# Optimization experiments

Hardware: AMD Instinct MI355X
Metric: run time of the kernel (lower is better)

## Reference

```python
import jax, jax.numpy as jnp
import numpy as np

EPS = 1e-12

def _safe_norm(x, axis):
    return jnp.sqrt(jnp.sum(x * x, axis=axis) + EPS)

def _forward(z, pos, edge_index, batch, batch_size, emb, centers, gamma,
             fw1, fb1, fw2, fb2, uw1, ub1, uw2, ub2,
             ew1, eb1, ew2, eb2, dipole_w, nac_w,
             aw1, ab1, aw2, ab2, yw1, yb1, yw2, yb2):
    row, col = edge_index[0], edge_index[1]
    N = pos.shape[0]
    diff = pos[col] - pos[row]                    # (E,3)
    dist = _safe_norm(diff, axis=1)               # (E,)
    dirs = diff / (dist[:, None] + 1e-8)          # (E,3)
    rbf = jnp.exp(-gamma * (dist[:, None] - centers) ** 2)   # (E,R)
    s = emb[z]                                    # (N,F)
    v = jnp.zeros((N, s.shape[1], 3), s.dtype)    # (N,F,3)
    n_layers = fw1.shape[0]
    for l in range(n_layers):
        # filter MLP on RBF features -> 3 gates per edge
        phi = jax.nn.silu(rbf @ fw1[l] + fb1[l]) @ fw2[l] + fb2[l]   # (E,3F)
        phi_ss, phi_vv, phi_sv = jnp.split(phi, 3, axis=-1)
        sc = s[col]                                                    # gather (E,F)
        m_s = jax.ops.segment_sum(phi_ss * sc, row, num_segments=N)    # (N,F)
        m_v_e = (phi_vv[..., None] * v[col]
                 + phi_sv[..., None] * dirs[:, None, :] * sc[..., None])  # (E,F,3)
        m_v = jax.ops.segment_sum(m_v_e, row, num_segments=N)          # (N,F,3)
        v_norm = _safe_norm(m_v, axis=-1)                              # (N,F)
        upd = (jax.nn.silu(jnp.concatenate([s, m_s, v_norm], axis=-1) @ uw1[l] + ub1[l])
               @ uw2[l] + ub2[l])                                       # (N,3F)
        delta_s, alpha, beta = jnp.split(upd, 3, axis=-1)
        s = s + delta_s
        v = alpha[..., None] * v + beta[..., None] * m_v
    # energy heads (stacked over states S)
    h = jax.nn.silu(jnp.einsum('nf,sfg->nsg', s, ew1) + eb1)           # (N,S,F)
    e_atom = (jnp.einsum('nsg,sgo->nso', h, ew2) + eb2)[..., 0]        # (N,S)
    energies = jax.ops.segment_sum(e_atom, batch, num_segments=batch_size)  # (M,S)
    dipoles = jax.ops.segment_sum(jnp.einsum('nfk,f->nk', v, dipole_w), batch,
                                  num_segments=batch_size)             # (M,3)
    nac = jax.ops.segment_sum(jnp.einsum('nfk,pf->npk', v, nac_w), batch,
                              num_segments=batch_size)                 # (M,P,3)
    gaps = energies[:, 1:] - energies[:, :1]                           # (M,S-1)
    lam = jax.nn.silu(gaps @ aw1 + ab1) @ aw2 + ab2                    # (M,1)
    nac_mag = _safe_norm(nac, axis=-1)                                 # (M,P)
    phi_y = jax.nn.sigmoid(
        jax.nn.silu(jnp.concatenate([gaps, nac_mag], axis=1) @ yw1 + yb1) @ yw2 + yb2)  # (M,1)
    return energies, dipoles, nac, lam, phi_y

N, E, F, R, L, S, M, A = 20000, 320000, 128, 20, 3, 4, 1000, 100
P = S - 1

def setup_inputs() -> dict:
    key = jax.random.key(0)
    ks = jax.random.split(key, 32)
    w = lambda i, shape, sc=0.05: jax.random.normal(ks[i], shape, jnp.float32) * sc
    return {
        'z': jax.random.randint(ks[0], (N,), 0, A),
        'pos': jax.random.normal(ks[1], (N, 3), jnp.float32),
        'edge_index': jax.random.randint(ks[2], (2, E), 0, N),
        'batch': jnp.sort(jax.random.randint(ks[3], (N,), 0, M)),
        'batch_size': M,
        'emb': jax.random.normal(ks[4], (A, F), jnp.float32),
        'centers': jnp.linspace(0.0, 5.0, R),
        'gamma': jnp.ones((R,), jnp.float32),
        'fw1': w(5, (L, R, F)), 'fb1': jnp.zeros((L, F)),
        'fw2': w(6, (L, F, 3 * F)), 'fb2': jnp.zeros((L, 3 * F)),
        'uw1': w(7, (L, 3 * F, F)), 'ub1': jnp.zeros((L, F)),
        'uw2': w(8, (L, F, 3 * F)), 'ub2': jnp.zeros((L, 3 * F)),
        'ew1': w(9, (S, F, F)), 'eb1': jnp.zeros((S, F)),
        'ew2': w(10, (S, F, 1)), 'eb2': jnp.zeros((S, 1)),
        'dipole_w': jax.random.normal(ks[11], (F,), jnp.float32),
        'nac_w': jax.random.normal(ks[12], (P, F), jnp.float32),
        'aw1': w(13, (S - 1, 64)), 'ab1': jnp.zeros((64,)),
        'aw2': w(14, (64, 1)), 'ab2': jnp.zeros((1,)),
        'yw1': w(15, (S - 1 + P, 128)), 'yb1': jnp.zeros((128,)),
        'yw2': w(16, (128, 1)), 'yb2': jnp.zeros((1,)),
    }

def reference(z, pos, edge_index, batch, batch_size, emb, centers, gamma,
              fw1, fb1, fw2, fb2, uw1, ub1, uw2, ub2,
              ew1, eb1, ew2, eb2, dipole_w, nac_w,
              aw1, ab1, aw2, ab2, yw1, yb1, yw2, yb2):
    return _forward(z, pos, edge_index, batch, batch_size, emb, centers, gamma,
                    fw1, fb1, fw2, fb2, uw1, ub1, uw2, ub2,
                    ew1, eb1, ew2, eb2, dipole_w, nac_w,
                    aw1, ab1, aw2, ab2, yw1, yb1, yw2, yb2)
```

## Files before the change

kernel.cpp:

```cpp
#include <hip/hip_runtime.h>
#include <hip/hip_fp16.h>

#define FDIM 128
#define RDIM 20

#define TAB_T 2048
#define TAB_RANGE 12.0f

constexpr int TH = 256;

__device__ __forceinline__ float siluf(float x) { return x / (1.f + __expf(-x)); }

__device__ __forceinline__ void store_h4(__half* p, float a, float b, float c, float d) {
    __half h[4] = {__float2half(a), __float2half(b), __float2half(c), __float2half(d)};
    *(uint2*)p = *(uint2*)h;
}

__global__ void k_init(const int* __restrict__ z, const float* __restrict__ emb,
                       float* __restrict__ s, __half* __restrict__ s_h, int N) {
    int i = blockIdx.x * blockDim.x + threadIdx.x;
    if (i >= N * FDIM) return;
    int n = i >> 7, f = i & 127;
    float val = emb[z[n] * FDIM + f];
    s[i] = val;
    s_h[i] = __float2half(val);
}

__global__ void k_hist(const int* __restrict__ erow, int* __restrict__ cursor, int E) {
    int e = blockIdx.x * blockDim.x + threadIdx.x;
    if (e < E) atomicAdd(&cursor[erow[e]], 1);
}

__global__ __launch_bounds__(256) void k_scan1(const int* __restrict__ cursor,
                                               int* __restrict__ rowstart,
                                               int* __restrict__ bsum, int N) {
    __shared__ int sh[256];
    int tid = threadIdx.x;
    int idx = blockIdx.x * 256 + tid;
    int x = (idx < N) ? cursor[idx] : 0;
    sh[tid] = x;
    __syncthreads();
    #pragma unroll
    for (int off = 1; off < 256; off <<= 1) {
        int t = (tid >= off) ? sh[tid - off] : 0;
        __syncthreads();
        sh[tid] += t;
        __syncthreads();
    }
    if (idx < N) rowstart[idx] = sh[tid] - x;
    if (tid == 255) bsum[blockIdx.x] = sh[255];
}

__global__ __launch_bounds__(256) void k_scan2(int* __restrict__ bsum,
                                               int* __restrict__ rowstart, int nb, int N) {
    __shared__ int sh[256];
    __shared__ int carry;
    int tid = threadIdx.x;
    if (tid == 0) carry = 0;
    __syncthreads();
    for (int base = 0; base < nb; base += 256) {
        int idx = base + tid;
        int x = (idx < nb) ? bsum[idx] : 0;
        sh[tid] = x;
        __syncthreads();
        #pragma unroll
        for (int off = 1; off < 256; off <<= 1) {
            int t = (tid >= off) ? sh[tid - off] : 0;
            __syncthreads();
            sh[tid] += t;
            __syncthreads();
        }
        if (idx < nb) bsum[idx] = carry + sh[tid] - x;
        __syncthreads();
        if (tid == 0) carry += sh[255];
        __syncthreads();
    }
    if (tid == 0) rowstart[N] = carry;
}

__global__ __launch_bounds__(256) void k_scan3(int* __restrict__ rowstart,
                                               int* __restrict__ cursor,
                                               const int* __restrict__ bsum, int N) {
    int idx = blockIdx.x * 256 + threadIdx.x;
    if (idx < N) {
        int val = rowstart[idx] + bsum[blockIdx.x];
        rowstart[idx] = val;
        cursor[idx] = val;
    }
}

__global__ void k_fill(const int* __restrict__ erow, int* __restrict__ cursor,
                       int* __restrict__ esort, int E) {
    int e = blockIdx.x * blockDim.x + threadIdx.x;
    if (e < E) {
        int p = atomicAdd(&cursor[erow[e]], 1);
        esort[p] = e;
    }
}

__global__ void k_geom(const float* __restrict__ pos, const int* __restrict__ erow,
                       const int* __restrict__ ecol, const int* __restrict__ esort,
                       int2* __restrict__ geo_ci, float4* __restrict__ geo_wd,
                       float inv_step, int E) {
    int i = blockIdx.x * blockDim.x + threadIdx.x;
    if (i >= E) return;
    int e  = esort[i];
    int rw = erow[e], cl = ecol[e];
    float dx = pos[cl*3+0] - pos[rw*3+0];
    float dy = pos[cl*3+1] - pos[rw*3+1];
    float dz = pos[cl*3+2] - pos[rw*3+2];
    float dist = sqrtf(dx*dx + dy*dy + dz*dz + 1e-12f);
    float inv = 1.f / (dist + 1e-8f);
    float u = fminf(dist * inv_step, (float)TAB_T);
    int t0 = min((int)u, TAB_T - 1);
    geo_ci[i] = make_int2(cl, t0);
    geo_wd[i] = make_float4(u - (float)t0, dx*inv, dy*inv, dz*inv);
}

__global__ __launch_bounds__(TH) void k_table(
    const float* __restrict__ centers, const float* __restrict__ gamma,
    const float* __restrict__ fw1b, const float* __restrict__ fb1b,
    const float* __restrict__ fw2b, const float* __restrict__ fb2b,
    __half* __restrict__ tabb, float step)
{
    __shared__ float sh_rbf[32][RDIM];
    __shared__ float sh_ht[FDIM][33];
    __shared__ float sh_w[32][3 * FDIM + 4];

    const int l   = blockIdx.y;
    const float* fw1 = fw1b + (size_t)l * RDIM * FDIM;
    const float* fb1 = fb1b + (size_t)l * FDIM;
    const float* fw2 = fw2b + (size_t)l * FDIM * 3 * FDIM;
    const float* fb2 = fb2b + (size_t)l * 3 * FDIM;
    __half* tab = tabb + (size_t)l * (TAB_T + 1) * 384;

    const int p0  = blockIdx.x * 32;
    const int tid = threadIdx.x;

    for (int i = tid; i < 32 * RDIM; i += TH) {
        int p = i / RDIM, r = i - p * RDIM;
        float d = (float)(p0 + p) * step - centers[r];
        sh_rbf[p][r] = __expf(-gamma[r] * d * d);
    }
    __syncthreads();
    for (int i = tid; i < 32 * FDIM; i += TH) {
        int p = i >> 7, f = i & 127;
        float acc = fb1[f];
        #pragma unroll
        for (int r = 0; r < RDIM; ++r) acc += sh_rbf[p][r] * fw1[r * FDIM + f];
        sh_ht[f][p] = siluf(acc);
    }

    const int eq = tid & 7;
    const int fq = tid >> 3;
    const int f0 = fq * 4;

    float pg[3][4][4];
    #pragma unroll
    for (int g3 = 0; g3 < 3; ++g3)
        #pragma unroll
        for (int ee = 0; ee < 4; ++ee)
            #pragma unroll
            for (int i = 0; i < 4; ++i) pg[g3][ee][i] = fb2[g3 * FDIM + f0 + i];

    const int kkr = tid >> 3;
    const int t8  = tid & 7;
    for (int kc = 0; kc < 4; ++kc) {
        __syncthreads();
        #pragma unroll
        for (int j = 0; j < 12; ++j) {
            int g = (t8 * 12 + j) * 4;
            float4 w4 = *(const float4*)&fw2[(size_t)(kc * 32 + kkr) * (3 * FDIM) + g];
            *(float4*)&sh_w[kkr][g] = w4;
        }
        __syncthreads();
        #pragma unroll 4
        for (int kk = 0; kk < 32; ++kk) {
            float hv[4];
            #pragma unroll
            for (int ee = 0; ee < 4; ++ee) hv[ee] = sh_ht[kc * 32 + kk][4 * eq + ee];
            #pragma unroll
            for (int g3 = 0; g3 < 3; ++g3) {
                float4 w4 = *(const float4*)&sh_w[kk][g3 * FDIM + f0];
                #pragma unroll
                for (int ee = 0; ee < 4; ++ee) {
                    pg[g3][ee][0] += hv[ee] * w4.x;
                    pg[g3][ee][1] += hv[ee] * w4.y;
                    pg[g3][ee][2] += hv[ee] * w4.z;
                    pg[g3][ee][3] += hv[ee] * w4.w;
                }
            }
        }
    }

    #pragma unroll
    for (int ee = 0; ee < 4; ++ee) {
        int pt = p0 + 4 * eq + ee;
        if (pt <= TAB_T) {
            #pragma unroll
            for (int g3 = 0; g3 < 3; ++g3)
                store_h4(&tab[(size_t)pt * 384 + g3 * FDIM + f0],
                         pg[g3][ee][0], pg[g3][ee][1], pg[g3][ee][2], pg[g3][ee][3]);
        }
    }
}

__global__ __launch_bounds__(256) void k_repack(const __half* __restrict__ tab,
                                                __half2* __restrict__ tab2) {
    int l = blockIdx.y;
    const __half* t  = tab  + (size_t)l * (TAB_T + 1) * 384;
    __half2*      t2 = tab2 + (size_t)l * TAB_T * 384;
    int i = blockIdx.x * 256 + threadIdx.x;
    t2[i] = __halves2half2(t[i], t[i + 384]);
}

__global__ __launch_bounds__(128) void k_gather(
    const int* __restrict__ rowstart,
    const int2* __restrict__ geo_ci, const float4* __restrict__ geo_wd,
    const __half2* __restrict__ tab2, const __half* __restrict__ s_h,
    const __half* __restrict__ v_h,
    __half* __restrict__ m_s_h, __half* __restrict__ vnorm_h, __half* __restrict__ m_v_h,
    int withv, int N)
{
    __shared__ int   sh_col[32];
    __shared__ int   sh_t0[32];
    __shared__ float sh_w[32];
    __shared__ float sh_d0[32], sh_d1[32], sh_d2[32];

    const int n   = blockIdx.x;
    const int tid = threadIdx.x;
    const int lo  = rowstart[n], hi = rowstart[n + 1];

    float acc_s = 0.f, av0 = 0.f, av1 = 0.f, av2 = 0.f;

    for (int base = lo; base < hi; base += 32) {
        const int ne = min(32, hi - base);
        __syncthreads();
        if (tid < 32) {
            int idx = base + tid;
            if (tid < ne) {
                int2   ci = geo_ci[idx];
                float4 wd = geo_wd[idx];
                sh_col[tid] = ci.x; sh_t0[tid] = ci.y;
                sh_w[tid] = wd.x;
                sh_d0[tid] = wd.y; sh_d1[tid] = wd.z; sh_d2[tid] = wd.w;
            } else {
                sh_col[tid] = 0; sh_t0[tid] = 0; sh_w[tid] = 0.f;
                sh_d0[tid] = sh_d1[tid] = sh_d2[tid] = 0.f;
            }
        }
        __syncthreads();
        if (withv) {
            #pragma unroll 2
            for (int el = 0; el < ne; ++el) {
                int   cl = sh_col[el];
                int   t0 = sh_t0[el];
                float w  = sh_w[el];
                const __half2* t2 = tab2 + (size_t)t0 * 384 + tid;
                float2 pss2 = __half22float2(t2[0]);
                float2 pvv2 = __half22float2(t2[128]);
                float2 psv2 = __half22float2(t2[256]);
                float pss = pss2.x + w * (pss2.y - pss2.x);
                float pvv = pvv2.x + w * (pvv2.y - pvv2.x);
                float psv = psv2.x + w * (psv2.y - psv2.x);
                float sc = __half2float(s_h[(size_t)cl * FDIM + tid]);
                const __half* vp = v_h + (size_t)cl * 3 * FDIM + tid;
                float svs = psv * sc;
                acc_s += pss * sc;
                av0 += pvv * __half2float(vp[0])        + svs * sh_d0[el];
                av1 += pvv * __half2float(vp[FDIM])     + svs * sh_d1[el];
                av2 += pvv * __half2float(vp[2*FDIM])   + svs * sh_d2[el];
            }
        } else {
            #pragma unroll 2
            for (int el = 0; el < ne; ++el) {
                int   cl = sh_col[el];
                int   t0 = sh_t0[el];
                float w  = sh_w[el];
                const __half2* t2 = tab2 + (size_t)t0 * 384 + tid;
                float2 pss2 = __half22float2(t2[0]);
                float2 psv2 = __half22float2(t2[256]);
                float pss = pss2.x + w * (pss2.y - pss2.x);
                float psv = psv2.x + w * (psv2.y - psv2.x);
                float sc = __half2float(s_h[(size_t)cl * FDIM + tid]);
                float svs = psv * sc;
                acc_s += pss * sc;
                av0 += svs * sh_d0[el];
                av1 += svs * sh_d1[el];
                av2 += svs * sh_d2[el];
            }
        }
    }

    m_s_h[(size_t)n * FDIM + tid]  = __float2half(acc_s);
    vnorm_h[(size_t)n * FDIM + tid] = __float2half(sqrtf(av0*av0 + av1*av1 + av2*av2 + 1e-12f));
    __half* mh = m_v_h + (size_t)n * 3 * FDIM + tid;
    mh[0]      = __float2half(av0);
    mh[FDIM]   = __float2half(av1);
    mh[2*FDIM] = __float2half(av2);
}

__global__ __launch_bounds__(256) void k_mlp1(
    const __half* __restrict__ s_h, const __half* __restrict__ m_s_h,
    const __half* __restrict__ vnorm_h,
    const float* __restrict__ uw1, const float* __restrict__ ub1,
    __half* __restrict__ u1_h, int N)
{
    __shared__ float shA[16][36];
    __shared__ float shB[16][132];

    const int tid = threadIdx.x;
    const int n0  = blockIdx.x * 32;
    const int tx  = tid & 15, ty = tid >> 4;
    const int cA  = tx * 4, cB = 64 + tx * 4;
    const int r0  = ty * 2;
    const int rs  = (tid & 127) >> 2;
    const int k4  = (tid & 3) * 4;
    const int bk  = tid >> 5;
    const int bc4 = (tid & 31) * 4;

    float acc[2][8];
    {
        float4 bA = *(const float4*)&ub1[cA];
        float4 bB = *(const float4*)&ub1[cB];
        #pragma unroll
        for (int i = 0; i < 2; ++i) {
            acc[i][0]=bA.x; acc[i][1]=bA.y; acc[i][2]=bA.z; acc[i][3]=bA.w;
            acc[i][4]=bB.x; acc[i][5]=bB.y; acc[i][6]=bB.z; acc[i][7]=bB.w;
        }
    }

    uint2 pa; float4 pb0, pb1;

#define MLP1_LOAD(kc) do { \
        pa = make_uint2(0u, 0u); \
        if (tid < 128) { \
            int kg = (kc) * 16 + k4; int n = n0 + rs; \
            if (n < N) { \
                const __half* base; \
                if (kg < 128)      base = &s_h[(size_t)n * FDIM + kg]; \
                else if (kg < 256) base = &m_s_h[(size_t)n * FDIM + kg - 128]; \
                else               base = &vnorm_h[(size_t)n * FDIM + kg - 256]; \
                pa = *(const uint2*)base; \
            } \
        } \
        pb0 = *(const float4*)&uw1[(size_t)((kc)*16 + bk) * FDIM + bc4]; \
        pb1 = *(const float4*)&uw1[(size_t)((kc)*16 + 8 + bk) * FDIM + bc4]; \
    } while (0)

    MLP1_LOAD(0);
    for (int kc = 0; kc < 24; ++kc) {
        __syncthreads();
        if (tid < 128) {
            const __half* ph = (const __half*)&pa;
            shA[k4+0][rs] = __half2float(ph[0]); shA[k4+1][rs] = __half2float(ph[1]);
            shA[k4+2][rs] = __half2float(ph[2]); shA[k4+3][rs] = __half2float(ph[3]);
        }
        *(float4*)&shB[bk][bc4]     = pb0;
        *(float4*)&shB[8 + bk][bc4] = pb1;
        if (kc + 1 < 24) MLP1_LOAD(kc + 1);
        __syncthreads();
        #pragma unroll
        for (int kk = 0; kk < 16; ++kk) {
            float2 a2 = *(const float2*)&shA[kk][r0];
            float4 b0 = *(const float4*)&shB[kk][cA];
            float4 b1 = *(const float4*)&shB[kk][cB];
            float av[2] = {a2.x, a2.y};
            #pragma unroll
            for (int i = 0; i < 2; ++i) {
                acc[i][0] += av[i]*b0.x; acc[i][1] += av[i]*b0.y;
                acc[i][2] += av[i]*b0.z; acc[i][3] += av[i]*b0.w;
                acc[i][4] += av[i]*b1.x; acc[i][5] += av[i]*b1.y;
                acc[i][6] += av[i]*b1.z; acc[i][7] += av[i]*b1.w;
            }
        }
    }
#undef MLP1_LOAD

    #pragma unroll
    for (int i = 0; i < 2; ++i) {
        int n = n0 + r0 + i;
        if (n < N) {
            store_h4(&u1_h[(size_t)n * FDIM + cA],
                     siluf(acc[i][0]), siluf(acc[i][1]), siluf(acc[i][2]), siluf(acc[i][3]));
            store_h4(&u1_h[(size_t)n * FDIM + cB],
                     siluf(acc[i][4]), siluf(acc[i][5]), siluf(acc[i][6]), siluf(acc[i][7]));
        }
    }
}

__global__ __launch_bounds__(256) void k_mlp2(
    const __half* __restrict__ u1_h, const float* __restrict__ uw2, const float* __restrict__ ub2,
    float* __restrict__ s, __half* __restrict__ v_h, const __half* __restrict__ m_v_h,
    __half* __restrict__ s_h, int wmirror, int N)
{
    __shared__ float shU[32][132];
    __shared__ float shB[16][132];

    const int tid = threadIdx.x;
    const int n0  = blockIdx.x * 32;
    const int tx  = tid & 15, ty = tid >> 4;
    const int cA  = tx * 4, cB = 64 + tx * 4;
    const int r0  = ty * 2;
    const int bk  = tid >> 5;
    const int bc4 = (tid & 31) * 4;

    #pragma unroll
    for (int it = 0; it < 2; ++it) {
        int idx = it * 256 + tid;
        int row = idx >> 4;
        int c4  = (idx & 15) * 8;
        int n = n0 + row;
        __half h[8];
        *(uint4*)h = make_uint4(0u,0u,0u,0u);
        if (n < N) *(uint4*)h = *(const uint4*)&u1_h[(size_t)n * FDIM + c4];
        #pragma unroll
        for (int j = 0; j < 8; ++j) shU[row][c4 + j] = __half2float(h[j]);
    }

    float4 pb0, pb1;
#define MLP2_LOADB(g, kc) do { \
        pb0 = *(const float4*)&uw2[(size_t)((kc)*16 + bk) * (3*FDIM) + (g) * FDIM + bc4]; \
        pb1 = *(const float4*)&uw2[(size_t)((kc)*16 + 8 + bk) * (3*FDIM) + (g) * FDIM + bc4]; \
    } while (0)

    MLP2_LOADB(0, 0);
    float alpha[2][8];

    for (int g = 0; g < 3; ++g) {
        float acc2[2][8];
        {
            float4 bA = *(const float4*)&ub2[g * FDIM + cA];
            float4 bB = *(const float4*)&ub2[g * FDIM + cB];
            #pragma unroll
            for (int i = 0; i < 2; ++i) {
                acc2[i][0]=bA.x; acc2[i][1]=bA.y; acc2[i][2]=bA.z; acc2[i][3]=bA.w;
                acc2[i][4]=bB.x; acc2[i][5]=bB.y; acc2[i][6]=bB.z; acc2[i][7]=bB.w;
            }
        }
        for (int kc = 0; kc < 8; ++kc) {
            __syncthreads();
            *(float4*)&shB[bk][bc4]     = pb0;
            *(float4*)&shB[8 + bk][bc4] = pb1;
            if (kc + 1 < 8)      MLP2_LOADB(g, kc + 1);
            else if (g + 1 < 3)  MLP2_LOADB(g + 1, 0);
            __syncthreads();
            #pragma unroll
            for (int kk = 0; kk < 16; ++kk) {
                int col = kc * 16 + kk;
                float4 b0 = *(const float4*)&shB[kk][cA];
                float4 b1 = *(const float4*)&shB[kk][cB];
                #pragma unroll
                for (int i = 0; i < 2; ++i) {
                    float uv = shU[r0 + i][col];
                    acc2[i][0] += uv*b0.x; acc2[i][1] += uv*b0.y;
                    acc2[i][2] += uv*b0.z; acc2[i][3] += uv*b0.w;
                    acc2[i][4] += uv*b1.x; acc2[i][5] += uv*b1.y;
                    acc2[i][6] += uv*b1.z; acc2[i][7] += uv*b1.w;
                }
            }
        }

        if (g == 0) {
            #pragma unroll
            for (int i = 0; i < 2; ++i) {
                int n = n0 + r0 + i;
                if (n < N) {
                    float4 s0 = *(const float4*)&s[(size_t)n * FDIM + cA];
                    float4 s1 = *(const float4*)&s[(size_t)n * FDIM + cB];
                    s0.x += acc2[i][0]; s0.y += acc2[i][1]; s0.z += acc2[i][2]; s0.w += acc2[i][3];
                    s1.x += acc2[i][4]; s1.y += acc2[i][5]; s1.z += acc2[i][6]; s1.w += acc2[i][7];
                    *(float4*)&s[(size_t)n * FDIM + cA] = s0;
                    *(float4*)&s[(size_t)n * FDIM + cB] = s1;
                    if (wmirror) {
                        store_h4(&s_h[(size_t)n * FDIM + cA], s0.x, s0.y, s0.z, s0.w);
                        store_h4(&s_h[(size_t)n * FDIM + cB], s1.x, s1.y, s1.z, s1.w);
                    }
                }
            }
        } else if (g == 1) {
            #pragma unroll
            for (int i = 0; i < 2; ++i)
                #pragma unroll
                for (int j = 0; j < 8; ++j) alpha[i][j] = acc2[i][j];
        } else {
            #pragma unroll
            for (int i = 0; i < 2; ++i) {
                int n = n0 + r0 + i;
                if (n < N) {
                    #pragma unroll
                    for (int k = 0; k < 3; ++k) {
                        __half* vhp = v_h + ((size_t)n * 3 + k) * FDIM;
                        const __half* mp = m_v_h + ((size_t)n * 3 + k) * FDIM;
                        __half vh[8], mh[8];
                        *(uint2*)&vh[0] = *(const uint2*)&vhp[cA];
                        *(uint2*)&vh[4] = *(const uint2*)&vhp[cB];
                        *(uint2*)&mh[0] = *(const uint2*)&mp[cA];
                        *(uint2*)&mh[4] = *(const uint2*)&mp[cB];
                        float nv[8];
                        #pragma unroll
                        for (int j = 0; j < 8; ++j)
                            nv[j] = alpha[i][j] * __half2float(vh[j])
                                  + acc2[i][j] * __half2float(mh[j]);
                        store_h4(&vhp[cA], nv[0], nv[1], nv[2], nv[3]);
                        store_h4(&vhp[cB], nv[4], nv[5], nv[6], nv[7]);
                    }
                }
            }
        }
    }
#undef MLP2_LOADB
}

__global__ __launch_bounds__(256) void k_energy2(
    const float* __restrict__ ew1, const float* __restrict__ eb1,
    const float* __restrict__ ew2, const float* __restrict__ eb2,
    const float* __restrict__ s, const int* __restrict__ batch,
    float* __restrict__ energies, int N, int S)
{
    __shared__ float shA[16][68];
    __shared__ float shB[16][132];

    const int tid = threadIdx.x;
    const int n0  = blockIdx.x * 64;
    const int st  = blockIdx.y;
    const int tx  = tid & 15, ty = tid >> 4;
    const int cA  = tx * 4, cB = 64 + tx * 4;
    const int r0  = ty * 4;
    const int rs  = tid >> 2;
    const int k4  = (tid & 3) * 4;

    float acc[4][8];
    {
        float4 bA = *(const float4*)&eb1[st * FDIM + cA];
        float4 bB = *(const float4*)&eb1[st * FDIM + cB];
        #pragma unroll
        for (int i = 0; i < 4; ++i) {
            acc[i][0]=bA.x; acc[i][1]=bA.y; acc[i][2]=bA.z; acc[i][3]=bA.w;
            acc[i][4]=bB.x; acc[i][5]=bB.y; acc[i][6]=bB.z; acc[i][7]=bB.w;
        }
    }

    for (int kc = 0; kc < 8; ++kc) {
        __syncthreads();
        {
            int kg = kc * 16 + k4;
            int n  = n0 + rs;
            float4 a = make_float4(0.f, 0.f, 0.f, 0.f);
            if (n < N) a = *(const float4*)&s[(size_t)n * FDIM + kg];
            shA[k4+0][rs] = a.x; shA[k4+1][rs] = a.y; shA[k4+2][rs] = a.z; shA[k4+3][rs] = a.w;
        }
        #pragma unroll
        for (int i = 0; i < 2; ++i) {
            int idx = tid + i * 256;
            int kk = idx >> 5;
            int c4 = (idx & 31) * 4;
            *(float4*)&shB[kk][c4] =
                *(const float4*)&ew1[(size_t)st * FDIM * FDIM + (size_t)(kc*16+kk) * FDIM + c4];
        }
        __syncthreads();
        #pragma unroll
        for (int kk = 0; kk < 16; ++kk) {
            float4 a4 = *(const float4*)&shA[kk][r0];
            float4 b0 = *(const float4*)&shB[kk][cA];
            float4 b1 = *(const float4*)&shB[kk][cB];
            float av[4] = {a4.x, a4.y, a4.z, a4.w};
            #pragma unroll
            for (int i = 0; i < 4; ++i) {
                acc[i][0] += av[i]*b0.x; acc[i][1] += av[i]*b0.y;
                acc[i][2] += av[i]*b0.z; acc[i][3] += av[i]*b0.w;
                acc[i][4] += av[i]*b1.x; acc[i][5] += av[i]*b1.y;
                acc[i][6] += av[i]*b1.z; acc[i][7] += av[i]*b1.w;
            }
        }
    }

    float4 wA = *(const float4*)&ew2[st * FDIM + cA];
    float4 wB = *(const float4*)&ew2[st * FDIM + cB];
    float p[4];
    #pragma unroll
    for (int i = 0; i < 4; ++i) {
        p[i]  = siluf(acc[i][0])*wA.x + siluf(acc[i][1])*wA.y
              + siluf(acc[i][2])*wA.z + siluf(acc[i][3])*wA.w;
        p[i] += siluf(acc[i][4])*wB.x + siluf(acc[i][5])*wB.y
              + siluf(acc[i][6])*wB.z + siluf(acc[i][7])*wB.w;
    }
    #pragma unroll
    for (int m = 1; m <= 8; m <<= 1) {
        #pragma unroll
        for (int i = 0; i < 4; ++i) p[i] += __shfl_xor(p[i], m, 64);
    }
    if (tx == 0) {
        float b2 = eb2[st];
        #pragma unroll
        for (int i = 0; i < 4; ++i) {
            int n = n0 + r0 + i;
            if (n < N) atomicAdd(&energies[batch[n] * S + st], p[i] + b2);
        }
    }
}

__global__ void k_vec(const __half* __restrict__ v_h, const float* __restrict__ dipole_w,
                      const float* __restrict__ nac_w, const int* __restrict__ batch,
                      float* __restrict__ dipoles, float* __restrict__ nac, int N)
{
    int n = blockIdx.x * 4 + (threadIdx.x >> 6);
    int lane = threadIdx.x & 63;
    if (n >= N) return;
    float pd[3] = {0.f, 0.f, 0.f};
    float pn[3][3] = {{0.f}};
    const __half* vb = v_h + (size_t)n * 3 * FDIM;
    for (int f = lane; f < FDIM; f += 64) {
        float v0 = __half2float(vb[f]);
        float v1 = __half2float(vb[FDIM + f]);
        float v2 = __half2float(vb[2*FDIM + f]);
        float wd = dipole_w[f];
        pd[0] += wd * v0; pd[1] += wd * v1; pd[2] += wd * v2;
        #pragma unroll
        for (int p = 0; p < 3; ++p) {
            float wn = nac_w[p * FDIM + f];
            pn[p][0] += wn * v0; pn[p][1] += wn * v1; pn[p][2] += wn * v2;
        }
    }
    #pragma unroll
    for (int d = 32; d > 0; d >>= 1) {
        #pragma unroll
        for (int k = 0; k < 3; ++k) pd[k] += __shfl_down(pd[k], d, 64);
        #pragma unroll
        for (int p = 0; p < 3; ++p)
            #pragma unroll
            for (int k = 0; k < 3; ++k) pn[p][k] += __shfl_down(pn[p][k], d, 64);
    }
    if (lane == 0) {
        int m = batch[n];
        #pragma unroll
        for (int k = 0; k < 3; ++k) atomicAdd(&dipoles[m * 3 + k], pd[k]);
        #pragma unroll
        for (int p = 0; p < 3; ++p)
            #pragma unroll
            for (int k = 0; k < 3; ++k) atomicAdd(&nac[(m * 3 + p) * 3 + k], pn[p][k]);
    }
}

__global__ __launch_bounds__(128) void k_heads(
    const float* __restrict__ aw1, const float* __restrict__ ab1,
    const float* __restrict__ aw2, const float* __restrict__ ab2,
    const float* __restrict__ yw1, const float* __restrict__ yb1,
    const float* __restrict__ yw2, const float* __restrict__ yb2,
    const float* __restrict__ energies, const float* __restrict__ nac,
    float* __restrict__ lam, float* __restrict__ phi_y, int M, int S)
{
    __shared__ float sh_in[8];
    __shared__ float sh_red[2];
    int m = blockIdx.x;
    if (m >= M) return;
    int tid = threadIdx.x;
    if (tid == 0) {
        float e0 = energies[m * S];
        for (int j = 0; j < 3; ++j) sh_in[j] = energies[m * S + 1 + j] - e0;
        for (int p = 0; p < 3; ++p) {
            float a = nac[(m * 3 + p) * 3 + 0];
            float b = nac[(m * 3 + p) * 3 + 1];
            float c = nac[(m * 3 + p) * 3 + 2];
            sh_in[3 + p] = sqrtf(a*a + b*b + c*c + 1e-12f);
        }
    }
    __syncthreads();
    float pa = 0.f;
    if (tid < 64) {
        float h = ab1[tid];
        #pragma unroll
        for (int j = 0; j < 3; ++j) h += sh_in[j] * aw1[j * 64 + tid];
        pa = siluf(h) * aw2[tid];
    }
    float h2 = yb1[tid];
    #pragma unroll
    for (int j = 0; j < 6; ++j) h2 += sh_in[j] * yw1[j * 128 + tid];
    float py = siluf(h2) * yw2[tid];
    #pragma unroll
    for (int d = 32; d > 0; d >>= 1) {
        pa += __shfl_down(pa, d, 64);
        py += __shfl_down(py, d, 64);
    }
    int wid = tid >> 6, lane = tid & 63;
    if (lane == 0) sh_red[wid] = py;
    __syncthreads();
    if (tid == 0) {
        lam[m] = pa + ab2[0];
        float yt = sh_red[0] + sh_red[1] + yb2[0];
        phi_y[m] = 1.f / (1.f + __expf(-yt));
    }
}

extern "C" void kernel_launch(void* const* d_in, const int* in_sizes, int n_in,
                              void* d_out, int out_size, void* d_ws, size_t ws_size,
                              hipStream_t stream)
{
    const int*   z        = (const int*)  d_in[0];
    const float* pos      = (const float*)d_in[1];
    const int*   eidx     = (const int*)  d_in[2];
    const int*   batch    = (const int*)  d_in[3];
    const float* emb      = (const float*)d_in[5];
    const float* centers  = (const float*)d_in[6];
    const float* gamma    = (const float*)d_in[7];
    const float* fw1      = (const float*)d_in[8];
    const float* fb1      = (const float*)d_in[9];
    const float* fw2      = (const float*)d_in[10];
    const float* fb2      = (const float*)d_in[11];
    const float* uw1      = (const float*)d_in[12];
    const float* ub1      = (const float*)d_in[13];
    const float* uw2      = (const float*)d_in[14];
    const float* ub2      = (const float*)d_in[15];
    const float* ew1      = (const float*)d_in[16];
    const float* eb1      = (const float*)d_in[17];
    const float* ew2      = (const float*)d_in[18];
    const float* eb2      = (const float*)d_in[19];
    const float* dipole_w = (const float*)d_in[20];
    const float* nac_w    = (const float*)d_in[21];
    const float* aw1      = (const float*)d_in[22];
    const float* ab1      = (const float*)d_in[23];
    const float* aw2      = (const float*)d_in[24];
    const float* ab2      = (const float*)d_in[25];
    const float* yw1      = (const float*)d_in[26];
    const float* yb1      = (const float*)d_in[27];
    const float* yw2      = (const float*)d_in[28];
    const float* yb2      = (const float*)d_in[29];

    const int N = in_sizes[0];
    const int E = in_sizes[2] / 2;
    const int S = in_sizes[19];
    const int P = in_sizes[21] / FDIM;
    const int L = in_sizes[9] / FDIM;
    const int M = out_size / (S + 3 + P * 3 + 2);

    const size_t NF = (size_t)N * FDIM;
    float*   s       = (float*)d_ws;
    __half*  s_h     = (__half*)(s + NF);
    __half*  v_h     = s_h + NF;
    __half*  m_s_h   = v_h + 3 * NF;
    __half*  vnorm_h = m_s_h + NF;
    __half*  m_v_h   = vnorm_h + NF;
    __half*  tab     = m_v_h + 3 * NF;
    __half2* tab2    = (__half2*)(tab + (size_t)L * (TAB_T + 1) * 384);
    float4*  geo_wd  = (float4*)(tab2 + (size_t)L * TAB_T * 384);
    int2*    geo_ci  = (int2*)(geo_wd + E);
    int* rowstart = (int*)(geo_ci + E);
    int* cursor   = rowstart + (N + 1);
    int* esort    = cursor + N;
    int* bsum     = esort + E;
    __half* u1_h = m_s_h;

    float* out      = (float*)d_out;
    float* energies = out;
    float* dipoles  = energies + (size_t)M * S;
    float* nac      = dipoles  + (size_t)M * 3;
    float* lam      = nac      + (size_t)M * P * 3;
    float* phi_y    = lam      + M;

    const int* erow = eidx;
    const int* ecol = eidx + E;

    const float step = TAB_RANGE / (float)TAB_T;
    const float inv_step = (float)TAB_T / TAB_RANGE;
    const int NB  = (N + 63) / 64;
    const int NB2 = (N + 31) / 32;
    const int NSB = (N + 255) / 256;

    hipMemsetAsync(d_out, 0, (size_t)out_size * sizeof(float), stream);
    hipMemsetAsync(cursor, 0, (size_t)N * sizeof(int), stream);
    hipMemsetAsync(v_h, 0, 3 * NF * sizeof(__half), stream);
    k_hist<<<(E + 255) / 256, 256, 0, stream>>>(erow, cursor, E);
    k_scan1<<<NSB, 256, 0, stream>>>(cursor, rowstart, bsum, N);
    k_scan2<<<1, 256, 0, stream>>>(bsum, rowstart, NSB, N);
    k_scan3<<<NSB, 256, 0, stream>>>(rowstart, cursor, bsum, N);
    k_fill<<<(E + 255) / 256, 256, 0, stream>>>(erow, cursor, esort, E);
    k_geom<<<(E + 255) / 256, 256, 0, stream>>>(pos, erow, ecol, esort, geo_ci, geo_wd, inv_step, E);
    k_init<<<(N * FDIM + 255) / 256, 256, 0, stream>>>(z, emb, s, s_h, N);

    const int tab_blocks = (TAB_T + 1 + 31) / 32;
    k_table<<<dim3(tab_blocks, L), TH, 0, stream>>>(centers, gamma, fw1, fb1, fw2, fb2, tab, step);
    k_repack<<<dim3(TAB_T * 384 / 256, L), 256, 0, stream>>>(tab, tab2);

    for (int l = 0; l < L; ++l) {
        const __half2* tab2_l = tab2 + (size_t)l * TAB_T * 384;
        k_gather<<<N, 128, 0, stream>>>(
            rowstart, geo_ci, geo_wd, tab2_l, s_h, v_h,
            m_s_h, vnorm_h, m_v_h, (l > 0) ? 1 : 0, N);
        k_mlp1<<<NB2, 256, 0, stream>>>(
            s_h, m_s_h, vnorm_h,
            uw1 + (size_t)l * 3 * FDIM * FDIM, ub1 + (size_t)l * FDIM, u1_h, N);
        k_mlp2<<<NB2, 256, 0, stream>>>(
            u1_h, uw2 + (size_t)l * FDIM * 3 * FDIM, ub2 + (size_t)l * 3 * FDIM,
            s, v_h, m_v_h, s_h, (l + 1 < L) ? 1 : 0, N);
    }

    k_energy2<<<dim3(NB, S), 256, 0, stream>>>(ew1, eb1, ew2, eb2, s, batch, energies, N, S);
    k_vec<<<(N + 3) / 4, 256, 0, stream>>>(v_h, dipole_w, nac_w, batch, dipoles, nac, N);
    k_heads<<<M, 128, 0, stream>>>(aw1, ab1, aw2, ab2, yw1, yb1, yw2, yb2,
                                   energies, nac, lam, phi_y, M, S);
}
```

Measured before the change: 612.2 us.

## Split update-MLP kernels across output column halves with 128-thread blocks

k_mlp1 and k_mlp2 now launch a 2D grid where blockIdx.y picks a 64-column half of the output. Each 128-thread block computes a 32x64 tile with 4x4 register blocking instead of a 32x128 tile with 2x8. This doubles the number of blocks to raise occupancy and parallelism for small N. Because the two column halves of mlp1 run concurrently and m_s_h is still being read by the other half, u1 moves to a separate workspace buffer instead of aliasing m_s_h. The cost is that the A operand tiles are loaded twice, and the workspace grows by one N x F half buffer.

```diff
diff --git a/kernel.cpp b/kernel.cpp
--- a/kernel.cpp
+++ b/kernel.cpp
@@ -300,33 +300,30 @@
     mh[2*FDIM] = __float2half(av2);
 }
 
-__global__ __launch_bounds__(256) void k_mlp1(
+__global__ __launch_bounds__(128) void k_mlp1(
     const __half* __restrict__ s_h, const __half* __restrict__ m_s_h,
     const __half* __restrict__ vnorm_h,
     const float* __restrict__ uw1, const float* __restrict__ ub1,
     __half* __restrict__ u1_h, int N)
 {
     __shared__ float shA[16][36];
-    __shared__ float shB[16][132];
+    __shared__ float shB[16][68];
 
     const int tid = threadIdx.x;
     const int n0  = blockIdx.x * 32;
+    const int cb  = blockIdx.y * 64;
     const int tx  = tid & 15, ty = tid >> 4;
-    const int cA  = tx * 4, cB = 64 + tx * 4;
-    const int r0  = ty * 2;
-    const int rs  = (tid & 127) >> 2;
+    const int cA  = tx * 4;
+    const int r0  = ty * 4;
+    const int rs  = tid >> 2;
     const int k4  = (tid & 3) * 4;
-    const int bk  = tid >> 5;
-    const int bc4 = (tid & 31) * 4;
-
-    float acc[2][8];
+
+    float acc[4][4];
     {
-        float4 bA = *(const float4*)&ub1[cA];
-        float4 bB = *(const float4*)&ub1[cB];
-        #pragma unroll
-        for (int i = 0; i < 2; ++i) {
-            acc[i][0]=bA.x; acc[i][1]=bA.y; acc[i][2]=bA.z; acc[i][3]=bA.w;
-            acc[i][4]=bB.x; acc[i][5]=bB.y; acc[i][6]=bB.z; acc[i][7]=bB.w;
+        float4 b4 = *(const float4*)&ub1[cb + cA];
+        #pragma unroll
+        for (int i = 0; i < 4; ++i) {
+            acc[i][0] = b4.x; acc[i][1] = b4.y; acc[i][2] = b4.z; acc[i][3] = b4.w;
         }
     }
 
@@ -334,176 +331,154 @@
 
 #define MLP1_LOAD(kc) do { \
         pa = make_uint2(0u, 0u); \
-        if (tid < 128) { \
-            int kg = (kc) * 16 + k4; int n = n0 + rs; \
-            if (n < N) { \
-                const __half* base; \
-                if (kg < 128)      base = &s_h[(size_t)n * FDIM + kg]; \
-                else if (kg < 256) base = &m_s_h[(size_t)n * FDIM + kg - 128]; \
-                else               base = &vnorm_h[(size_t)n * FDIM + kg - 256]; \
-                pa = *(const uint2*)base; \
-            } \
-        } \
-        pb0 = *(const float4*)&uw1[(size_t)((kc)*16 + bk) * FDIM + bc4]; \
-        pb1 = *(const float4*)&uw1[(size_t)((kc)*16 + 8 + bk) * FDIM + bc4]; \
+        { int kg = (kc) * 16 + k4; int n = n0 + rs; \
+          if (n < N) { \
+              const __half* base; \
+              if (kg < 128)      base = &s_h[(size_t)n * FDIM + kg]; \
+              else if (kg < 256) base = &m_s_h[(size_t)n * FDIM + kg - 128]; \
+              else               base = &vnorm_h[(size_t)n * FDIM + kg - 256]; \
+              pa = *(const uint2*)base; } } \
+        pb0 = *(const float4*)&uw1[(size_t)((kc)*16 + ty) * FDIM + cb + cA]; \
+        pb1 = *(const float4*)&uw1[(size_t)((kc)*16 + 8 + ty) * FDIM + cb + cA]; \
     } while (0)
 
     MLP1_LOAD(0);
     for (int kc = 0; kc < 24; ++kc) {
         __syncthreads();
-        if (tid < 128) {
+        {
             const __half* ph = (const __half*)&pa;
             shA[k4+0][rs] = __half2float(ph[0]); shA[k4+1][rs] = __half2float(ph[1]);
             shA[k4+2][rs] = __half2float(ph[2]); shA[k4+3][rs] = __half2float(ph[3]);
-        }
-        *(float4*)&shB[bk][bc4]     = pb0;
-        *(float4*)&shB[8 + bk][bc4] = pb1;
+            *(float4*)&shB[ty][cA]     = pb0;
+            *(float4*)&shB[8 + ty][cA] = pb1;
+        }
         if (kc + 1 < 24) MLP1_LOAD(kc + 1);
         __syncthreads();
         #pragma unroll
         for (int kk = 0; kk < 16; ++kk) {
-            float2 a2 = *(const float2*)&shA[kk][r0];
-            float4 b0 = *(const float4*)&shB[kk][cA];
-            float4 b1 = *(const float4*)&shB[kk][cB];
-            float av[2] = {a2.x, a2.y};
-            #pragma unroll
-            for (int i = 0; i < 2; ++i) {
-                acc[i][0] += av[i]*b0.x; acc[i][1] += av[i]*b0.y;
-                acc[i][2] += av[i]*b0.z; acc[i][3] += av[i]*b0.w;
-                acc[i][4] += av[i]*b1.x; acc[i][5] += av[i]*b1.y;
-                acc[i][6] += av[i]*b1.z; acc[i][7] += av[i]*b1.w;
+            float4 a4 = *(const float4*)&shA[kk][r0];
+            float4 b4 = *(const float4*)&shB[kk][cA];
+            float av[4] = {a4.x, a4.y, a4.z, a4.w};
+            #pragma unroll
+            for (int i = 0; i < 4; ++i) {
+                acc[i][0] += av[i]*b4.x; acc[i][1] += av[i]*b4.y;
+                acc[i][2] += av[i]*b4.z; acc[i][3] += av[i]*b4.w;
             }
         }
     }
 #undef MLP1_LOAD
 
     #pragma unroll
-    for (int i = 0; i < 2; ++i) {
+    for (int i = 0; i < 4; ++i) {
         int n = n0 + r0 + i;
         if (n < N) {
-            store_h4(&u1_h[(size_t)n * FDIM + cA],
+            store_h4(&u1_h[(size_t)n * FDIM + cb + cA],
                      siluf(acc[i][0]), siluf(acc[i][1]), siluf(acc[i][2]), siluf(acc[i][3]));
-            store_h4(&u1_h[(size_t)n * FDIM + cB],
-                     siluf(acc[i][4]), siluf(acc[i][5]), siluf(acc[i][6]), siluf(acc[i][7]));
-        }
-    }
-}
-
-__global__ __launch_bounds__(256) void k_mlp2(
+        }
+    }
+}
+
+__global__ __launch_bounds__(128) void k_mlp2(
     const __half* __restrict__ u1_h, const float* __restrict__ uw2, const float* __restrict__ ub2,
     float* __restrict__ s, __half* __restrict__ v_h, const __half* __restrict__ m_v_h,
     __half* __restrict__ s_h, int wmirror, int N)
 {
     __shared__ float shU[32][132];
-    __shared__ float shB[16][132];
+    __shared__ float shB[16][68];
 
     const int tid = threadIdx.x;
     const int n0  = blockIdx.x * 32;
+    const int cb  = blockIdx.y * 64;
     const int tx  = tid & 15, ty = tid >> 4;
-    const int cA  = tx * 4, cB = 64 + tx * 4;
-    const int r0  = ty * 2;
-    const int bk  = tid >> 5;
-    const int bc4 = (tid & 31) * 4;
-
-    #pragma unroll
-    for (int it = 0; it < 2; ++it) {
-        int idx = it * 256 + tid;
+    const int cA  = tx * 4;
+    const int r0  = ty * 4;
+
+    #pragma unroll
+    for (int it = 0; it < 4; ++it) {
+        int idx = it * 128 + tid;
         int row = idx >> 4;
-        int c4  = (idx & 15) * 8;
+        int c8  = (idx & 15) * 8;
         int n = n0 + row;
         __half h[8];
         *(uint4*)h = make_uint4(0u,0u,0u,0u);
-        if (n < N) *(uint4*)h = *(const uint4*)&u1_h[(size_t)n * FDIM + c4];
-        #pragma unroll
-        for (int j = 0; j < 8; ++j) shU[row][c4 + j] = __half2float(h[j]);
+        if (n < N) *(uint4*)h = *(const uint4*)&u1_h[(size_t)n * FDIM + c8];
+        #pragma unroll
+        for (int j = 0; j < 8; ++j) shU[row][c8 + j] = __half2float(h[j]);
     }
 
     float4 pb0, pb1;
 #define MLP2_LOADB(g, kc) do { \
-        pb0 = *(const float4*)&uw2[(size_t)((kc)*16 + bk) * (3*FDIM) + (g) * FDIM + bc4]; \
-        pb1 = *(const float4*)&uw2[(size_t)((kc)*16 + 8 + bk) * (3*FDIM) + (g) * FDIM + bc4]; \
+        pb0 = *(const float4*)&uw2[(size_t)((kc)*16 + ty) * (3*FDIM) + (g) * FDIM + cb + cA]; \
+        pb1 = *(const float4*)&uw2[(size_t)((kc)*16 + 8 + ty) * (3*FDIM) + (g) * FDIM + cb + cA]; \
     } while (0)
 
     MLP2_LOADB(0, 0);
-    float alpha[2][8];
+    float alpha[4][4];
 
     for (int g = 0; g < 3; ++g) {
-        float acc2[2][8];
+        float acc2[4][4];
         {
-            float4 bA = *(const float4*)&ub2[g * FDIM + cA];
-            float4 bB = *(const float4*)&ub2[g * FDIM + cB];
-            #pragma unroll
-            for (int i = 0; i < 2; ++i) {
-                acc2[i][0]=bA.x; acc2[i][1]=bA.y; acc2[i][2]=bA.z; acc2[i][3]=bA.w;
-                acc2[i][4]=bB.x; acc2[i][5]=bB.y; acc2[i][6]=bB.z; acc2[i][7]=bB.w;
+            float4 b4 = *(const float4*)&ub2[g * FDIM + cb + cA];
+            #pragma unroll
+            for (int i = 0; i < 4; ++i) {
+                acc2[i][0]=b4.x; acc2[i][1]=b4.y; acc2[i][2]=b4.z; acc2[i][3]=b4.w;
             }
         }
         for (int kc = 0; kc < 8; ++kc) {
             __syncthreads();
-            *(float4*)&shB[bk][bc4]     = pb0;
-            *(float4*)&shB[8 + bk][bc4] = pb1;
+            *(float4*)&shB[ty][cA]     = pb0;
+            *(float4*)&shB[8 + ty][cA] = pb1;
             if (kc + 1 < 8)      MLP2_LOADB(g, kc + 1);
             else if (g + 1 < 3)  MLP2_LOADB(g + 1, 0);
             __syncthreads();
             #pragma unroll
             for (int kk = 0; kk < 16; ++kk) {
                 int col = kc * 16 + kk;
-                float4 b0 = *(const float4*)&shB[kk][cA];
-                float4 b1 = *(const float4*)&shB[kk][cB];
+                float4 b4 = *(const float4*)&shB[kk][cA];
                 #pragma unroll
-                for (int i = 0; i < 2; ++i) {
+                for (int i = 0; i < 4; ++i) {
                     float uv = shU[r0 + i][col];
-                    acc2[i][0] += uv*b0.x; acc2[i][1] += uv*b0.y;
-                    acc2[i][2] += uv*b0.z; acc2[i][3] += uv*b0.w;
-                    acc2[i][4] += uv*b1.x; acc2[i][5] += uv*b1.y;
-                    acc2[i][6] += uv*b1.z; acc2[i][7] += uv*b1.w;
+                    acc2[i][0] += uv*b4.x; acc2[i][1] += uv*b4.y;
+                    acc2[i][2] += uv*b4.z; acc2[i][3] += uv*b4.w;
                 }
             }
         }
 
         if (g == 0) {
             #pragma unroll
-            for (int i = 0; i < 2; ++i) {
+            for (int i = 0; i < 4; ++i) {
                 int n = n0 + r0 + i;
                 if (n < N) {
-                    float4 s0 = *(const float4*)&s[(size_t)n * FDIM + cA];
-                    float4 s1 = *(const float4*)&s[(size_t)n * FDIM + cB];
+                    float4 s0 = *(const float4*)&s[(size_t)n * FDIM + cb + cA];
                     s0.x += acc2[i][0]; s0.y += acc2[i][1]; s0.z += acc2[i][2]; s0.w += acc2[i][3];
-                    s1.x += acc2[i][4]; s1.y += acc2[i][5]; s1.z += acc2[i][6]; s1.w += acc2[i][7];
-                    *(float4*)&s[(size_t)n * FDIM + cA] = s0;
-                    *(float4*)&s[(size_t)n * FDIM + cB] = s1;
-                    if (wmirror) {
-                        store_h4(&s_h[(size_t)n * FDIM + cA], s0.x, s0.y, s0.z, s0.w);
-                        store_h4(&s_h[(size_t)n * FDIM + cB], s1.x, s1.y, s1.z, s1.w);
-                    }
+                    *(float4*)&s[(size_t)n * FDIM + cb + cA] = s0;
+                    if (wmirror)
+                        store_h4(&s_h[(size_t)n * FDIM + cb + cA], s0.x, s0.y, s0.z, s0.w);
                 }
             }
         } else if (g == 1) {
             #pragma unroll
-            for (int i = 0; i < 2; ++i)
+            for (int i = 0; i < 4; ++i)
                 #pragma unroll
-                for (int j = 0; j < 8; ++j) alpha[i][j] = acc2[i][j];
+                for (int j = 0; j < 4; ++j) alpha[i][j] = acc2[i][j];
         } else {
             #pragma unroll
-            for (int i = 0; i < 2; ++i) {
+            for (int i = 0; i < 4; ++i) {
                 int n = n0 + r0 + i;
                 if (n < N) {
                     #pragma unroll
                     for (int k = 0; k < 3; ++k) {
-                        __half* vhp = v_h + ((size_t)n * 3 + k) * FDIM;
-                        const __half* mp = m_v_h + ((size_t)n * 3 + k) * FDIM;
-                        __half vh[8], mh[8];
-                        *(uint2*)&vh[0] = *(const uint2*)&vhp[cA];
-                        *(uint2*)&vh[4] = *(const uint2*)&vhp[cB];
-                        *(uint2*)&mh[0] = *(const uint2*)&mp[cA];
-                        *(uint2*)&mh[4] = *(const uint2*)&mp[cB];
-                        float nv[8];
+                        __half* vhp = v_h + ((size_t)n * 3 + k) * FDIM + cb + cA;
+                        const __half* mp = m_v_h + ((size_t)n * 3 + k) * FDIM + cb + cA;
+                        __half vh[4], mh[4];
+                        *(uint2*)vh = *(const uint2*)vhp;
+                        *(uint2*)mh = *(const uint2*)mp;
+                        float nv[4];
                         #pragma unroll
-                        for (int j = 0; j < 8; ++j)
+                        for (int j = 0; j < 4; ++j)
                             nv[j] = alpha[i][j] * __half2float(vh[j])
                                   + acc2[i][j] * __half2float(mh[j]);
-                        store_h4(&vhp[cA], nv[0], nv[1], nv[2], nv[3]);
-                        store_h4(&vhp[cB], nv[4], nv[5], nv[6], nv[7]);
+                        store_h4(vhp, nv[0], nv[1], nv[2], nv[3]);
                     }
                 }
             }
@@ -740,7 +715,8 @@
     __half*  m_s_h   = v_h + 3 * NF;
     __half*  vnorm_h = m_s_h + NF;
     __half*  m_v_h   = vnorm_h + NF;
-    __half*  tab     = m_v_h + 3 * NF;
+    __half*  u1_hb   = m_v_h + 3 * NF;
+    __half*  tab     = u1_hb + NF;
     __half2* tab2    = (__half2*)(tab + (size_t)L * (TAB_T + 1) * 384);
     float4*  geo_wd  = (float4*)(tab2 + (size_t)L * TAB_T * 384);
     int2*    geo_ci  = (int2*)(geo_wd + E);
@@ -748,7 +724,6 @@
     int* cursor   = rowstart + (N + 1);
     int* esort    = cursor + N;
     int* bsum     = esort + E;
-    __half* u1_h = m_s_h;
 
     float* out      = (float*)d_out;
     float* energies = out;
@@ -786,11 +761,11 @@
         k_gather<<<N, 128, 0, stream>>>(
             rowstart, geo_ci, geo_wd, tab2_l, s_h, v_h,
             m_s_h, vnorm_h, m_v_h, (l > 0) ? 1 : 0, N);
-        k_mlp1<<<NB2, 256, 0, stream>>>(
+        k_mlp1<<<dim3(NB2, 2), 128, 0, stream>>>(
             s_h, m_s_h, vnorm_h,
-            uw1 + (size_t)l * 3 * FDIM * FDIM, ub1 + (size_t)l * FDIM, u1_h, N);
-        k_mlp2<<<NB2, 256, 0, stream>>>(
-            u1_h, uw2 + (size_t)l * FDIM * 3 * FDIM, ub2 + (size_t)l * 3 * FDIM,
+            uw1 + (size_t)l * 3 * FDIM * FDIM, ub1 + (size_t)l * FDIM, u1_hb, N);
+        k_mlp2<<<dim3(NB2, 2), 128, 0, stream>>>(
+            u1_hb, uw2 + (size_t)l * FDIM * 3 * FDIM, ub2 + (size_t)l * 3 * FDIM,
             s, v_h, m_v_h, s_h, (l + 1 < L) ? 1 : 0, N);
     }
 
```

Result: faster. 557.6 us (-8.9%).
